# Optimization experiments

Hardware: AMD Instinct MI355X
Metric: run time of the kernel (lower is better)

Reference implementation:

```python
import jax, jax.numpy as jnp
import numpy as np

B, C, T = 128, 9, 2048
R = T // 4            # reduced_timesteps after two MaxPool1d(2)
N = B * R             # total graph nodes
E_SINGLE = 8192       # edges per sample graph (avg degree 16 over R nodes)
HID = 128
OUT = 12


def setup_inputs():
    key = jax.random.key(0)
    ks = jax.random.split(key, 14)
    x = jax.random.normal(ks[0], (B, C, T), jnp.float32)
    # per-sample graph, replicated with offset i*R per batch element (as in forward)
    single = jax.random.randint(ks[1], (2, E_SINGLE), 0, R)
    offsets = (jnp.arange(B) * R)[None, :, None]
    edge_index = (single[:, None, :] + offsets).reshape(2, -1)  # [2, B*E_SINGLE]

    def lin(k, fan_in, shape):
        return jax.random.normal(k, shape, jnp.float32) / np.sqrt(fan_in)

    return {
        "x": x,
        "edge_index": edge_index,
        "conv1_w": lin(ks[2], C * 5, (16, C, 5)),
        "conv1_b": jnp.zeros((16,), jnp.float32),
        "conv2_w": lin(ks[3], 16 * 5, (32, 16, 5)),
        "conv2_b": jnp.zeros((32,), jnp.float32),
        "gcn1_w": lin(ks[4], 32, (32, HID)),
        "gcn1_b": jnp.zeros((HID,), jnp.float32),
        "gcn2_w": lin(ks[5], HID, (HID, HID)),
        "gcn2_b": jnp.zeros((HID,), jnp.float32),
        "fc_w": lin(ks[6], HID, (HID, OUT)),
        "fc_b": jnp.zeros((OUT,), jnp.float32),
    }


def _gcn_conv(h, edge_index, w, b, n):
    # PyG GCNConv: linear -> add self-loops -> sym-normalized sum aggregation -> + bias
    h = h @ w
    loops = jnp.arange(n)
    row = jnp.concatenate([edge_index[0], loops])  # source
    col = jnp.concatenate([edge_index[1], loops])  # target (aggregation)
    deg = jax.ops.segment_sum(jnp.ones(col.shape, h.dtype), col, num_segments=n)
    dis = jnp.where(deg > 0, jax.lax.rsqrt(jnp.maximum(deg, 1e-12)), 0.0)
    norm = dis[row] * dis[col]                      # [E+N]
    out = jax.ops.segment_sum(norm[:, None] * h[row], col, num_segments=n)
    return out + b


def _temporal_conv(x, w1, b1, w2, b2):
    dn = ("NCH", "OIH", "NCH")
    h = jax.lax.conv_general_dilated(x, w1, (1,), [(2, 2)], dimension_numbers=dn)
    h = jax.nn.relu(h + b1[None, :, None])
    h = jax.lax.reduce_window(h, -jnp.inf, jax.lax.max, (1, 1, 2), (1, 1, 2), "VALID")
    h = jax.lax.conv_general_dilated(h, w2, (1,), [(2, 2)], dimension_numbers=dn)
    h = jax.nn.relu(h + b2[None, :, None])
    h = jax.lax.reduce_window(h, -jnp.inf, jax.lax.max, (1, 1, 2), (1, 1, 2), "VALID")
    return h  # [B, 32, R]


def reference(x, edge_index, conv1_w, conv1_b, conv2_w, conv2_b,
              gcn1_w, gcn1_b, gcn2_w, gcn2_b, fc_w, fc_b):
    h = _temporal_conv(x, conv1_w, conv1_b, conv2_w, conv2_b)   # [B, 32, R]
    nodes = h.transpose(0, 2, 1).reshape(B * R, 32)             # [N, 32]
    g = jax.nn.relu(_gcn_conv(nodes, edge_index, gcn1_w, gcn1_b, N))
    g = jax.nn.relu(_gcn_conv(g, edge_index, gcn2_w, gcn2_b, N))
    g = g.reshape(B, R, HID).mean(axis=1)                       # [B, HID]
    return g @ fc_w + fc_b                                      # [B, OUT]
```

## Files before the change

kernel.cpp:

```cpp
#include <hip/hip_runtime.h>
#include <hip/hip_bf16.h>

#define BB   128
#define CIN  9
#define TT   2048
#define RR   512
#define NN   (BB*RR)
#define HID  128
#define NOUT 12

typedef __attribute__((ext_vector_type(8))) short short8;
typedef __attribute__((ext_vector_type(4))) float f32x4;

static __device__ inline unsigned short f2bf(float f) {
    unsigned int u = __float_as_uint(f);
    unsigned int r = (u + 0x7fffu + ((u >> 16) & 1u)) >> 16;
    return (unsigned short)r;
}
static __device__ inline float bf2f(unsigned short u) {
    return __uint_as_float(((unsigned int)u) << 16);
}

__global__ __launch_bounds__(512) void k_convs(const float* __restrict__ x,
        const float* __restrict__ w1, const float* __restrict__ b1,
        const float* __restrict__ w2, const float* __restrict__ b2,
        float* __restrict__ nodes,
        const int* __restrict__ ei, int E, int es,
        int* __restrict__ rptr, float* __restrict__ dis, int* __restrict__ adj) {
    __shared__ float sx[CIN][268];
    __shared__ float s1[16][132];
    __shared__ int lcnt[512];
    __shared__ int sp[512];
    __shared__ int lcur[512];
    int tid = threadIdx.x;

    if (blockIdx.x == 0) {
        int t = tid;
        lcnt[t] = 0;
        __syncthreads();
        for (int i = t; i < es; i += 512) atomicAdd(&lcnt[ei[E + i]], 1);
        __syncthreads();
        int c = lcnt[t];
        sp[t] = c;
        __syncthreads();
        for (int off = 1; off < 512; off <<= 1) {
            int v = sp[t];
            int add = (t >= off) ? sp[t - off] : 0;
            __syncthreads();
            sp[t] = v + add;
            __syncthreads();
        }
        int excl = sp[t] - c;
        rptr[t] = excl;
        if (t == 511) rptr[512] = es;
        dis[t] = rsqrtf((float)c + 1.0f);
        lcur[t] = excl;
        __syncthreads();
        for (int i = t; i < es; i += 512) {
            int row = ei[i], col = ei[E + i];
            int pos = atomicAdd(&lcur[col], 1);
            adj[pos] = row;
        }
        return;
    }

    int cb = blockIdx.x - 1;
    int b  = cb >> 3;
    int r0 = (cb & 7) * 64;
    int wv   = __builtin_amdgcn_readfirstlane(tid >> 6);
    int lane = tid & 63;

    for (int idx = tid; idx < CIN * 268; idx += 512) {
        int c = idx / 268, j = idx - c * 268;
        int g = 4 * r0 - 6 + j;
        float v = 0.f;
        if (g >= 0 && g < TT) v = x[(b * CIN + c) * TT + g];
        sx[c][j] = v;
    }
    __syncthreads();

    {
        int c1a = wv * 2, c1b = wv * 2 + 1;
        float biasA = b1[c1a], biasB = b1[c1b];
        for (int pp = lane; pp < 132; pp += 64) {
            int p = 2 * r0 - 2 + pp;
            float valA = 0.f, valB = 0.f;
            if (p >= 0 && p < 1024) {
                float a0A = biasA, a1A = biasA, a0B = biasB, a1B = biasB;
#pragma unroll
                for (int c = 0; c < CIN; ++c) {
                    const float2* px = (const float2*)&sx[c][2 * pp];
                    float2 q0 = px[0], q1 = px[1], q2 = px[2];
                    {
                        const float* wp = &w1[(c1a * CIN + c) * 5];
                        float k0 = wp[0], k1 = wp[1], k2 = wp[2], k3 = wp[3], k4 = wp[4];
                        a0A += q0.x*k0 + q0.y*k1 + q1.x*k2 + q1.y*k3 + q2.x*k4;
                        a1A += q0.y*k0 + q1.x*k1 + q1.y*k2 + q2.x*k3 + q2.y*k4;
                    }
                    {
                        const float* wp = &w1[(c1b * CIN + c) * 5];
                        float k0 = wp[0], k1 = wp[1], k2 = wp[2], k3 = wp[3], k4 = wp[4];
                        a0B += q0.x*k0 + q0.y*k1 + q1.x*k2 + q1.y*k3 + q2.x*k4;
                        a1B += q0.y*k0 + q1.x*k1 + q1.y*k2 + q2.x*k3 + q2.y*k4;
                    }
                }
                valA = fmaxf(fmaxf(a0A, a1A), 0.f);
                valB = fmaxf(fmaxf(a0B, a1B), 0.f);
            }
            s1[c1a][pp] = valA;
            s1[c1b][pp] = valB;
        }
    }
    __syncthreads();

    int rl = lane;
    float acc0[4], acc1[4];
#pragma unroll
    for (int o = 0; o < 4; ++o) {
        float bv = b2[wv * 4 + o];
        acc0[o] = bv; acc1[o] = bv;
    }
#pragma unroll
    for (int c = 0; c < 16; ++c) {
        const float2* ps = (const float2*)&s1[c][2 * rl];
        float2 q0 = ps[0], q1 = ps[1], q2 = ps[2];
#pragma unroll
        for (int o = 0; o < 4; ++o) {
            const float* wp = &w2[((wv * 4 + o) * 16 + c) * 5];
            float k0 = wp[0], k1 = wp[1], k2 = wp[2], k3 = wp[3], k4 = wp[4];
            acc0[o] += q0.x*k0 + q0.y*k1 + q1.x*k2 + q1.y*k3 + q2.x*k4;
            acc1[o] += q0.y*k0 + q1.x*k1 + q1.y*k2 + q2.x*k3 + q2.y*k4;
        }
    }
    int n = b * RR + r0 + rl;
    float4 ov;
    ov.x = fmaxf(fmaxf(acc0[0], acc1[0]), 0.f);
    ov.y = fmaxf(fmaxf(acc0[1], acc1[1]), 0.f);
    ov.z = fmaxf(fmaxf(acc0[2], acc1[2]), 0.f);
    ov.w = fmaxf(fmaxf(acc0[3], acc1[3]), 0.f);
    *(float4*)&nodes[n * 32 + wv * 4] = ov;
}

__global__ __launch_bounds__(256) void k_gl1(const int* __restrict__ rptr,
        const int* __restrict__ adj, const float* __restrict__ dis,
        const float* __restrict__ nodes, const float* __restrict__ w,
        const float* __restrict__ bias, unsigned short* __restrict__ h16) {
    __shared__ float srow[32][32];
    __shared__ float sw[32 * 128];
    int bid = (blockIdx.x & 7) * 256 + (blockIdx.x >> 3);
    int tid = threadIdx.x;
    int nbase = bid * 32;
    int b = nbase >> 9;
    const float* hb = nodes + (size_t)b * RR * 32;

    {
        const float4* src = (const float4*)w;
        float4* dst = (float4*)sw;
#pragma unroll
        for (int i = 0; i < 4; ++i) dst[tid + i * 256] = src[tid + i * 256];
    }

    int ln   = tid >> 3;
    int lane = tid & 7;
    int r = (nbase & 511) + ln;
    int s = rptr[r], e = rptr[r + 1];
    float dn = dis[r];
    float4 acc = make_float4(0.f, 0.f, 0.f, 0.f);
    for (int base = s; base < e; base += 8) {
        int j = base + lane;
        int src = 0; float nd = 0.f;
        if (j < e) { src = adj[j]; nd = dis[src]; }
        int cnt = min(8, e - base);
        int k = 0;
        for (; k + 4 <= cnt; k += 4) {
            int   s0 = __shfl(src, k, 8),     s1 = __shfl(src, k + 1, 8);
            int   s2 = __shfl(src, k + 2, 8), s3 = __shfl(src, k + 3, 8);
            float n0 = __shfl(nd, k, 8),      n1 = __shfl(nd, k + 1, 8);
            float n2 = __shfl(nd, k + 2, 8),  n3 = __shfl(nd, k + 3, 8);
            float4 v0 = *(const float4*)&hb[(size_t)s0 * 32 + lane * 4];
            float4 v1 = *(const float4*)&hb[(size_t)s1 * 32 + lane * 4];
            float4 v2 = *(const float4*)&hb[(size_t)s2 * 32 + lane * 4];
            float4 v3 = *(const float4*)&hb[(size_t)s3 * 32 + lane * 4];
            float w0 = dn * n0, w1 = dn * n1, w2 = dn * n2, w3 = dn * n3;
            acc.x += w0*v0.x + w1*v1.x + w2*v2.x + w3*v3.x;
            acc.y += w0*v0.y + w1*v1.y + w2*v2.y + w3*v3.y;
            acc.z += w0*v0.z + w1*v1.z + w2*v2.z + w3*v3.z;
            acc.w += w0*v0.w + w1*v1.w + w2*v2.w + w3*v3.w;
        }
        for (; k < cnt; ++k) {
            int   sk = __shfl(src, k, 8);
            float nk = __shfl(nd, k, 8);
            float4 v = *(const float4*)&hb[(size_t)sk * 32 + lane * 4];
            float wgt = dn * nk;
            acc.x += wgt * v.x; acc.y += wgt * v.y;
            acc.z += wgt * v.z; acc.w += wgt * v.w;
        }
    }
    {
        float4 v = *(const float4*)&hb[(size_t)r * 32 + lane * 4];
        float wgt = dn * dn;
        acc.x += wgt * v.x; acc.y += wgt * v.y;
        acc.z += wgt * v.z; acc.w += wgt * v.w;
    }
    *(float4*)&srow[ln][lane * 4] = acc;
    __syncthreads();

    int fq = tid & 31;
    int ng = tid >> 5;
    float a[4][4];
#pragma unroll
    for (int j = 0; j < 4; ++j)
#pragma unroll
        for (int q = 0; q < 4; ++q) a[j][q] = 0.f;
#pragma unroll
    for (int c = 0; c < 32; ++c) {
        float4 wvv = *(const float4*)&sw[c * 128 + fq * 4];
#pragma unroll
        for (int j = 0; j < 4; ++j) {
            float xc = srow[ng * 4 + j][c];
            a[j][0] += xc * wvv.x; a[j][1] += xc * wvv.y;
            a[j][2] += xc * wvv.z; a[j][3] += xc * wvv.w;
        }
    }
    float4 bv = *(const float4*)&bias[fq * 4];
#pragma unroll
    for (int j = 0; j < 4; ++j) {
        ushort4 o;
        o.x = f2bf(fmaxf(a[j][0] + bv.x, 0.f));
        o.y = f2bf(fmaxf(a[j][1] + bv.y, 0.f));
        o.z = f2bf(fmaxf(a[j][2] + bv.z, 0.f));
        o.w = f2bf(fmaxf(a[j][3] + bv.w, 0.f));
        *(ushort4*)&h16[(size_t)(nbase + ng * 4 + j) * 128 + fq * 4] = o;
    }
}

__global__ __launch_bounds__(256) void k_lin2(const unsigned short* __restrict__ g16,
        const float* __restrict__ w, unsigned short* __restrict__ h16) {
    __shared__ unsigned short srow[64][136];
    __shared__ unsigned short swT[128][136];
    int tid = threadIdx.x;
    int nbase = blockIdx.x * 64;

    {
        const ushort4* src = (const ushort4*)(g16 + (size_t)nbase * 128);
#pragma unroll
        for (int i = 0; i < 8; ++i) {
            int idx = tid + i * 256;
            int row = idx >> 5, col4 = idx & 31;
            ushort4 v = src[idx];
            *(ushort4*)&srow[row][col4 * 4] = v;
        }
    }
    {
        for (int i = 0; i < 64; ++i) {
            int idx = i * 256 + tid;
            int c = idx >> 7, f = idx & 127;
            swT[f][c] = f2bf(w[idx]);
        }
    }
    __syncthreads();

    int wv  = tid >> 6;
    int lane = tid & 63;
    int m0 = wv * 16;
    int l15 = lane & 15;
    int quad = lane >> 4;
    f32x4 acc[8];
#pragma unroll
    for (int nt = 0; nt < 8; ++nt) acc[nt] = (f32x4){0.f, 0.f, 0.f, 0.f};
#pragma unroll
    for (int kc = 0; kc < 4; ++kc) {
        int k0 = kc * 32 + quad * 8;
        short8 a = *(const short8*)&srow[m0 + l15][k0];
#pragma unroll
        for (int nt = 0; nt < 8; ++nt) {
            short8 b = *(const short8*)&swT[nt * 16 + l15][k0];
            acc[nt] = __builtin_amdgcn_mfma_f32_16x16x32_bf16(a, b, acc[nt], 0, 0, 0);
        }
    }
#pragma unroll
    for (int nt = 0; nt < 8; ++nt) {
#pragma unroll
        for (int r = 0; r < 4; ++r) {
            int row = m0 + quad * 4 + r;
            int col = nt * 16 + l15;
            h16[(size_t)(nbase + row) * 128 + col] = f2bf(acc[nt][r]);
        }
    }
}

__global__ __launch_bounds__(256) void k_gather128(const int* __restrict__ rptr,
        const int* __restrict__ adj, const float* __restrict__ dis,
        const unsigned short* __restrict__ h, const float* __restrict__ bias,
        float* __restrict__ partial) {
    __shared__ float sred[8][128];
    int bid  = (blockIdx.x & 7) * 1024 + (blockIdx.x >> 3);
    int tid  = threadIdx.x;
    int g    = tid >> 5;
    int lane = tid & 31;
    int node = bid * 8 + g;
    int b = node >> 9;
    int r = node & 511;
    const unsigned short* hb = h + (size_t)b * RR * 128;
    int s = rptr[r], e = rptr[r + 1];
    float dn = dis[r];
    float4 acc = make_float4(0.f, 0.f, 0.f, 0.f);
    for (int base = s; base < e; base += 32) {
        int j = base + lane;
        int src = 0; float nd = 0.f;
        if (j < e) { src = adj[j]; nd = dis[src]; }
        int cnt = min(32, e - base);
        int k = 0;
        for (; k + 4 <= cnt; k += 4) {
            int   s0 = __shfl(src, k, 32),     s1 = __shfl(src, k + 1, 32);
            int   s2 = __shfl(src, k + 2, 32), s3 = __shfl(src, k + 3, 32);
            float n0 = __shfl(nd, k, 32),      n1 = __shfl(nd, k + 1, 32);
            float n2 = __shfl(nd, k + 2, 32),  n3 = __shfl(nd, k + 3, 32);
            ushort4 u0 = *(const ushort4*)&hb[(size_t)s0 * 128 + lane * 4];
            ushort4 u1 = *(const ushort4*)&hb[(size_t)s1 * 128 + lane * 4];
            ushort4 u2 = *(const ushort4*)&hb[(size_t)s2 * 128 + lane * 4];
            ushort4 u3 = *(const ushort4*)&hb[(size_t)s3 * 128 + lane * 4];
            float w0 = dn * n0, w1 = dn * n1, w2 = dn * n2, w3 = dn * n3;
            acc.x += w0*bf2f(u0.x) + w1*bf2f(u1.x) + w2*bf2f(u2.x) + w3*bf2f(u3.x);
            acc.y += w0*bf2f(u0.y) + w1*bf2f(u1.y) + w2*bf2f(u2.y) + w3*bf2f(u3.y);
            acc.z += w0*bf2f(u0.z) + w1*bf2f(u1.z) + w2*bf2f(u2.z) + w3*bf2f(u3.z);
            acc.w += w0*bf2f(u0.w) + w1*bf2f(u1.w) + w2*bf2f(u2.w) + w3*bf2f(u3.w);
        }
        for (; k < cnt; ++k) {
            int   sk = __shfl(src, k, 32);
            float nk = __shfl(nd, k, 32);
            ushort4 u = *(const ushort4*)&hb[(size_t)sk * 128 + lane * 4];
            float wgt = dn * nk;
            acc.x += wgt * bf2f(u.x); acc.y += wgt * bf2f(u.y);
            acc.z += wgt * bf2f(u.z); acc.w += wgt * bf2f(u.w);
        }
    }
    ushort4 u = *(const ushort4*)&hb[(size_t)r * 128 + lane * 4];
    float wgt = dn * dn;
    float4 bv = *(const float4*)&bias[lane * 4];
    acc.x = fmaxf(acc.x + wgt * bf2f(u.x) + bv.x, 0.f);
    acc.y = fmaxf(acc.y + wgt * bf2f(u.y) + bv.y, 0.f);
    acc.z = fmaxf(acc.z + wgt * bf2f(u.z) + bv.z, 0.f);
    acc.w = fmaxf(acc.w + wgt * bf2f(u.w) + bv.w, 0.f);
    *(float4*)&sred[g][lane * 4] = acc;
    __syncthreads();
    if (tid < 128) {
        float ssum = 0.f;
#pragma unroll
        for (int j = 0; j < 8; ++j) ssum += sred[j][tid];
        partial[(size_t)bid * 128 + tid] = ssum;
    }
}

__global__ __launch_bounds__(128) void k_fc(const float* __restrict__ partial,
        const float* __restrict__ fw, const float* __restrict__ fb,
        float* __restrict__ out) {
    __shared__ float sm[HID];
    int b = blockIdx.x, f = threadIdx.x;
    float acc = 0.f;
#pragma unroll 8
    for (int j = 0; j < 64; ++j) acc += partial[(size_t)(b * 64 + j) * 128 + f];
    sm[f] = acc * (1.0f / RR);
    __syncthreads();
    if (f < NOUT) {
        float s = fb[f];
#pragma unroll
        for (int c = 0; c < HID; ++c) s += sm[c] * fw[c * NOUT + f];
        out[b * NOUT + f] = s;
    }
}

extern "C" void kernel_launch(void* const* d_in, const int* in_sizes, int n_in,
                              void* d_out, int out_size, void* d_ws, size_t ws_size,
                              hipStream_t stream) {
    const float* x   = (const float*)d_in[0];
    const int*   ei  = (const int*)d_in[1];
    const float* c1w = (const float*)d_in[2];
    const float* c1b = (const float*)d_in[3];
    const float* c2w = (const float*)d_in[4];
    const float* c2b = (const float*)d_in[5];
    const float* g1w = (const float*)d_in[6];
    const float* g1b = (const float*)d_in[7];
    const float* g2w = (const float*)d_in[8];
    const float* g2b = (const float*)d_in[9];
    const float* fw  = (const float*)d_in[10];
    const float* fb  = (const float*)d_in[11];
    float* out = (float*)d_out;
    int E  = in_sizes[1] / 2;
    int es = E / BB;

    char* ws = (char*)d_ws;
    float*          nodes   = (float*)(ws);
    unsigned short* bufA16  = (unsigned short*)(ws + (8u  << 20));
    unsigned short* bufC16  = (unsigned short*)(ws + (24u << 20));
    int*   rptr    = (int*)  (ws + (40u << 20));
    float* dis     = (float*)(ws + (40u << 20) + 4096);
    int*   adj     = (int*)  (ws + (40u << 20) + 8192);
    float* partial = (float*)(ws + (41u << 20));

    k_convs<<<BB * 8 + 1, 512, 0, stream>>>(x, c1w, c1b, c2w, c2b, nodes,
                                            ei, E, es, rptr, dis, adj);

    k_gl1<<<NN / 32, 256, 0, stream>>>(rptr, adj, dis, nodes, g1w, g1b, bufA16);

    k_lin2<<<NN / 64, 256, 0, stream>>>(bufA16, g2w, bufC16);
    k_gather128<<<NN / 8, 256, 0, stream>>>(rptr, adj, dis, bufC16, g2b, partial);

    k_fc<<<BB, 128, 0, stream>>>(partial, fw, fb, out);
}
```

Baseline: 172.9 us.

## Fuse GCN layer-2 linear into layer-1 kernel and store conv nodes in bf16

Merges the separate layer-2 linear kernel into the layer-1 aggregate+linear kernel. The 32-node layer-1 outputs stay in shared memory and feed bf16 MFMAs directly, which removes a full N×128 bf16 round trip through global memory and one launch. The second-layer weight is transposed to bf16 once, in the graph-building block of the conv kernel. Conv outputs are now stored as bf16, halving gather traffic for layer 1, at some cost in precision. The layer-2 gather loop also gets an 8-wide unroll, and the MFMA B operand is read from global memory (L2) rather than LDS.

```diff
diff --git a/kernel.cpp b/kernel.cpp
--- a/kernel.cpp
+++ b/kernel.cpp
@@ -21,12 +21,15 @@
     return __uint_as_float(((unsigned int)u) << 16);
 }
 
+#define MFMA16(a, b, c) __builtin_amdgcn_mfma_f32_16x16x32_bf16((a), (b), (c), 0, 0, 0)
+
 __global__ __launch_bounds__(512) void k_convs(const float* __restrict__ x,
         const float* __restrict__ w1, const float* __restrict__ b1,
         const float* __restrict__ w2, const float* __restrict__ b2,
-        float* __restrict__ nodes,
+        unsigned short* __restrict__ nodes16,
         const int* __restrict__ ei, int E, int es,
-        int* __restrict__ rptr, float* __restrict__ dis, int* __restrict__ adj) {
+        int* __restrict__ rptr, float* __restrict__ dis, int* __restrict__ adj,
+        const float* __restrict__ g2w, unsigned short* __restrict__ w2t) {
     __shared__ float sx[CIN][268];
     __shared__ float s1[16][132];
     __shared__ int lcnt[512];
@@ -60,6 +63,10 @@
             int row = ei[i], col = ei[E + i];
             int pos = atomicAdd(&lcur[col], 1);
             adj[pos] = row;
+        }
+        for (int idx = t; idx < 128 * 128; idx += 512) {
+            int c2 = idx >> 7, f = idx & 127;
+            w2t[f * 128 + c2] = f2bf(g2w[idx]);
         }
         return;
     }
@@ -133,25 +140,27 @@
         }
     }
     int n = b * RR + r0 + rl;
-    float4 ov;
-    ov.x = fmaxf(fmaxf(acc0[0], acc1[0]), 0.f);
-    ov.y = fmaxf(fmaxf(acc0[1], acc1[1]), 0.f);
-    ov.z = fmaxf(fmaxf(acc0[2], acc1[2]), 0.f);
-    ov.w = fmaxf(fmaxf(acc0[3], acc1[3]), 0.f);
-    *(float4*)&nodes[n * 32 + wv * 4] = ov;
-}
-
-__global__ __launch_bounds__(256) void k_gl1(const int* __restrict__ rptr,
+    ushort4 ov;
+    ov.x = f2bf(fmaxf(fmaxf(acc0[0], acc1[0]), 0.f));
+    ov.y = f2bf(fmaxf(fmaxf(acc0[1], acc1[1]), 0.f));
+    ov.z = f2bf(fmaxf(fmaxf(acc0[2], acc1[2]), 0.f));
+    ov.w = f2bf(fmaxf(fmaxf(acc0[3], acc1[3]), 0.f));
+    *(ushort4*)&nodes16[n * 32 + wv * 4] = ov;
+}
+
+__global__ __launch_bounds__(256) void k_gl12(const int* __restrict__ rptr,
         const int* __restrict__ adj, const float* __restrict__ dis,
-        const float* __restrict__ nodes, const float* __restrict__ w,
-        const float* __restrict__ bias, unsigned short* __restrict__ h16) {
+        const unsigned short* __restrict__ nodes16, const float* __restrict__ w,
+        const float* __restrict__ bias, const unsigned short* __restrict__ w2t,
+        unsigned short* __restrict__ h2out) {
+    __shared__ float sw[32 * 128];
     __shared__ float srow[32][32];
-    __shared__ float sw[32 * 128];
+    __shared__ unsigned short sh1[32][136];
     int bid = (blockIdx.x & 7) * 256 + (blockIdx.x >> 3);
     int tid = threadIdx.x;
     int nbase = bid * 32;
     int b = nbase >> 9;
-    const float* hb = nodes + (size_t)b * RR * 32;
+    const unsigned short* hb = nodes16 + (size_t)b * RR * 32;
 
     {
         const float4* src = (const float4*)w;
@@ -160,14 +169,14 @@
         for (int i = 0; i < 4; ++i) dst[tid + i * 256] = src[tid + i * 256];
     }
 
-    int ln   = tid >> 3;
-    int lane = tid & 7;
+    int ln    = tid >> 3;
+    int lane8 = tid & 7;
     int r = (nbase & 511) + ln;
     int s = rptr[r], e = rptr[r + 1];
     float dn = dis[r];
     float4 acc = make_float4(0.f, 0.f, 0.f, 0.f);
     for (int base = s; base < e; base += 8) {
-        int j = base + lane;
+        int j = base + lane8;
         int src = 0; float nd = 0.f;
         if (j < e) { src = adj[j]; nd = dis[src]; }
         int cnt = min(8, e - base);
@@ -177,114 +186,93 @@
             int   s2 = __shfl(src, k + 2, 8), s3 = __shfl(src, k + 3, 8);
             float n0 = __shfl(nd, k, 8),      n1 = __shfl(nd, k + 1, 8);
             float n2 = __shfl(nd, k + 2, 8),  n3 = __shfl(nd, k + 3, 8);
-            float4 v0 = *(const float4*)&hb[(size_t)s0 * 32 + lane * 4];
-            float4 v1 = *(const float4*)&hb[(size_t)s1 * 32 + lane * 4];
-            float4 v2 = *(const float4*)&hb[(size_t)s2 * 32 + lane * 4];
-            float4 v3 = *(const float4*)&hb[(size_t)s3 * 32 + lane * 4];
+            ushort4 u0 = *(const ushort4*)&hb[(size_t)s0 * 32 + lane8 * 4];
+            ushort4 u1 = *(const ushort4*)&hb[(size_t)s1 * 32 + lane8 * 4];
+            ushort4 u2 = *(const ushort4*)&hb[(size_t)s2 * 32 + lane8 * 4];
+            ushort4 u3 = *(const ushort4*)&hb[(size_t)s3 * 32 + lane8 * 4];
             float w0 = dn * n0, w1 = dn * n1, w2 = dn * n2, w3 = dn * n3;
-            acc.x += w0*v0.x + w1*v1.x + w2*v2.x + w3*v3.x;
-            acc.y += w0*v0.y + w1*v1.y + w2*v2.y + w3*v3.y;
-            acc.z += w0*v0.z + w1*v1.z + w2*v2.z + w3*v3.z;
-            acc.w += w0*v0.w + w1*v1.w + w2*v2.w + w3*v3.w;
+            acc.x += w0*bf2f(u0.x) + w1*bf2f(u1.x) + w2*bf2f(u2.x) + w3*bf2f(u3.x);
+            acc.y += w0*bf2f(u0.y) + w1*bf2f(u1.y) + w2*bf2f(u2.y) + w3*bf2f(u3.y);
+            acc.z += w0*bf2f(u0.z) + w1*bf2f(u1.z) + w2*bf2f(u2.z) + w3*bf2f(u3.z);
+            acc.w += w0*bf2f(u0.w) + w1*bf2f(u1.w) + w2*bf2f(u2.w) + w3*bf2f(u3.w);
         }
         for (; k < cnt; ++k) {
             int   sk = __shfl(src, k, 8);
             float nk = __shfl(nd, k, 8);
-            float4 v = *(const float4*)&hb[(size_t)sk * 32 + lane * 4];
+            ushort4 u = *(const ushort4*)&hb[(size_t)sk * 32 + lane8 * 4];
             float wgt = dn * nk;
-            acc.x += wgt * v.x; acc.y += wgt * v.y;
-            acc.z += wgt * v.z; acc.w += wgt * v.w;
+            acc.x += wgt * bf2f(u.x); acc.y += wgt * bf2f(u.y);
+            acc.z += wgt * bf2f(u.z); acc.w += wgt * bf2f(u.w);
         }
     }
     {
-        float4 v = *(const float4*)&hb[(size_t)r * 32 + lane * 4];
+        ushort4 u = *(const ushort4*)&hb[(size_t)r * 32 + lane8 * 4];
         float wgt = dn * dn;
-        acc.x += wgt * v.x; acc.y += wgt * v.y;
-        acc.z += wgt * v.z; acc.w += wgt * v.w;
-    }
-    *(float4*)&srow[ln][lane * 4] = acc;
-    __syncthreads();
-
-    int fq = tid & 31;
-    int ng = tid >> 5;
-    float a[4][4];
-#pragma unroll
-    for (int j = 0; j < 4; ++j)
-#pragma unroll
-        for (int q = 0; q < 4; ++q) a[j][q] = 0.f;
-#pragma unroll
-    for (int c = 0; c < 32; ++c) {
-        float4 wvv = *(const float4*)&sw[c * 128 + fq * 4];
+        acc.x += wgt * bf2f(u.x); acc.y += wgt * bf2f(u.y);
+        acc.z += wgt * bf2f(u.z); acc.w += wgt * bf2f(u.w);
+    }
+    *(float4*)&srow[ln][lane8 * 4] = acc;
+    __syncthreads();
+
+    {
+        int fq = tid & 31;
+        int ng = tid >> 5;
+        float a[4][4];
+#pragma unroll
+        for (int j = 0; j < 4; ++j)
+#pragma unroll
+            for (int q = 0; q < 4; ++q) a[j][q] = 0.f;
+#pragma unroll
+        for (int c = 0; c < 32; ++c) {
+            float4 wvv = *(const float4*)&sw[c * 128 + fq * 4];
+#pragma unroll
+            for (int j = 0; j < 4; ++j) {
+                float xc = srow[ng * 4 + j][c];
+                a[j][0] += xc * wvv.x; a[j][1] += xc * wvv.y;
+                a[j][2] += xc * wvv.z; a[j][3] += xc * wvv.w;
+            }
+        }
+        float4 bv = *(const float4*)&bias[fq * 4];
 #pragma unroll
         for (int j = 0; j < 4; ++j) {
-            float xc = srow[ng * 4 + j][c];
-            a[j][0] += xc * wvv.x; a[j][1] += xc * wvv.y;
-            a[j][2] += xc * wvv.z; a[j][3] += xc * wvv.w;
-        }
-    }
-    float4 bv = *(const float4*)&bias[fq * 4];
-#pragma unroll
-    for (int j = 0; j < 4; ++j) {
-        ushort4 o;
-        o.x = f2bf(fmaxf(a[j][0] + bv.x, 0.f));
-        o.y = f2bf(fmaxf(a[j][1] + bv.y, 0.f));
-        o.z = f2bf(fmaxf(a[j][2] + bv.z, 0.f));
-        o.w = f2bf(fmaxf(a[j][3] + bv.w, 0.f));
-        *(ushort4*)&h16[(size_t)(nbase + ng * 4 + j) * 128 + fq * 4] = o;
-    }
-}
-
-__global__ __launch_bounds__(256) void k_lin2(const unsigned short* __restrict__ g16,
-        const float* __restrict__ w, unsigned short* __restrict__ h16) {
-    __shared__ unsigned short srow[64][136];
-    __shared__ unsigned short swT[128][136];
-    int tid = threadIdx.x;
-    int nbase = blockIdx.x * 64;
+            ushort4 o;
+            o.x = f2bf(fmaxf(a[j][0] + bv.x, 0.f));
+            o.y = f2bf(fmaxf(a[j][1] + bv.y, 0.f));
+            o.z = f2bf(fmaxf(a[j][2] + bv.z, 0.f));
+            o.w = f2bf(fmaxf(a[j][3] + bv.w, 0.f));
+            *(ushort4*)&sh1[ng * 4 + j][fq * 4] = o;
+        }
+    }
+    __syncthreads();
 
     {
-        const ushort4* src = (const ushort4*)(g16 + (size_t)nbase * 128);
-#pragma unroll
-        for (int i = 0; i < 8; ++i) {
-            int idx = tid + i * 256;
-            int row = idx >> 5, col4 = idx & 31;
-            ushort4 v = src[idx];
-            *(ushort4*)&srow[row][col4 * 4] = v;
-        }
-    }
-    {
-        for (int i = 0; i < 64; ++i) {
-            int idx = i * 256 + tid;
-            int c = idx >> 7, f = idx & 127;
-            swT[f][c] = f2bf(w[idx]);
-        }
-    }
-    __syncthreads();
-
-    int wv  = tid >> 6;
-    int lane = tid & 63;
-    int m0 = wv * 16;
-    int l15 = lane & 15;
-    int quad = lane >> 4;
-    f32x4 acc[8];
-#pragma unroll
-    for (int nt = 0; nt < 8; ++nt) acc[nt] = (f32x4){0.f, 0.f, 0.f, 0.f};
-#pragma unroll
-    for (int kc = 0; kc < 4; ++kc) {
-        int k0 = kc * 32 + quad * 8;
-        short8 a = *(const short8*)&srow[m0 + l15][k0];
-#pragma unroll
-        for (int nt = 0; nt < 8; ++nt) {
-            short8 b = *(const short8*)&swT[nt * 16 + l15][k0];
-            acc[nt] = __builtin_amdgcn_mfma_f32_16x16x32_bf16(a, b, acc[nt], 0, 0, 0);
-        }
-    }
-#pragma unroll
-    for (int nt = 0; nt < 8; ++nt) {
-#pragma unroll
-        for (int r = 0; r < 4; ++r) {
-            int row = m0 + quad * 4 + r;
-            int col = nt * 16 + l15;
-            h16[(size_t)(nbase + row) * 128 + col] = f2bf(acc[nt][r]);
+        int wv   = tid >> 6;
+        int lane = tid & 63;
+        int l15  = lane & 15;
+        int quad = lane >> 4;
+        int m0 = (wv & 1) * 16;
+        int nh = wv >> 1;
+        f32x4 acc2[4];
+#pragma unroll
+        for (int nt = 0; nt < 4; ++nt) acc2[nt] = (f32x4){0.f, 0.f, 0.f, 0.f};
+#pragma unroll
+        for (int kc = 0; kc < 4; ++kc) {
+            short8 a = *(const short8*)&sh1[m0 + l15][kc * 32 + quad * 8];
+#pragma unroll
+            for (int nt = 0; nt < 4; ++nt) {
+                int col0 = nh * 64 + nt * 16;
+                short8 bfr = *(const short8*)&w2t[(size_t)(col0 + l15) * 128 + kc * 32 + quad * 8];
+                acc2[nt] = MFMA16(a, bfr, acc2[nt]);
+            }
+        }
+#pragma unroll
+        for (int nt = 0; nt < 4; ++nt) {
+            int col = nh * 64 + nt * 16 + l15;
+#pragma unroll
+            for (int rr2 = 0; rr2 < 4; ++rr2) {
+                int row = nbase + m0 + quad * 4 + rr2;
+                h2out[(size_t)row * 128 + col] = f2bf(acc2[nt][rr2]);
+            }
         }
     }
 }
@@ -311,6 +299,25 @@
         if (j < e) { src = adj[j]; nd = dis[src]; }
         int cnt = min(32, e - base);
         int k = 0;
+        for (; k + 8 <= cnt; k += 8) {
+#pragma unroll
+            for (int uu = 0; uu < 2; ++uu) {
+                int kk = k + uu * 4;
+                int   s0 = __shfl(src, kk, 32),     s1 = __shfl(src, kk + 1, 32);
+                int   s2 = __shfl(src, kk + 2, 32), s3 = __shfl(src, kk + 3, 32);
+                float n0 = __shfl(nd, kk, 32),      n1 = __shfl(nd, kk + 1, 32);
+                float n2 = __shfl(nd, kk + 2, 32),  n3 = __shfl(nd, kk + 3, 32);
+                ushort4 u0 = *(const ushort4*)&hb[(size_t)s0 * 128 + lane * 4];
+                ushort4 u1 = *(const ushort4*)&hb[(size_t)s1 * 128 + lane * 4];
+                ushort4 u2 = *(const ushort4*)&hb[(size_t)s2 * 128 + lane * 4];
+                ushort4 u3 = *(const ushort4*)&hb[(size_t)s3 * 128 + lane * 4];
+                float w0 = dn * n0, w1 = dn * n1, w2 = dn * n2, w3 = dn * n3;
+                acc.x += w0*bf2f(u0.x) + w1*bf2f(u1.x) + w2*bf2f(u2.x) + w3*bf2f(u3.x);
+                acc.y += w0*bf2f(u0.y) + w1*bf2f(u1.y) + w2*bf2f(u2.y) + w3*bf2f(u3.y);
+                acc.z += w0*bf2f(u0.z) + w1*bf2f(u1.z) + w2*bf2f(u2.z) + w3*bf2f(u3.z);
+                acc.w += w0*bf2f(u0.w) + w1*bf2f(u1.w) + w2*bf2f(u2.w) + w3*bf2f(u3.w);
+            }
+        }
         for (; k + 4 <= cnt; k += 4) {
             int   s0 = __shfl(src, k, 32),     s1 = __shfl(src, k + 1, 32);
             int   s2 = __shfl(src, k + 2, 32), s3 = __shfl(src, k + 3, 32);
@@ -390,20 +397,19 @@
     int es = E / BB;
 
     char* ws = (char*)d_ws;
-    float*          nodes   = (float*)(ws);
-    unsigned short* bufA16  = (unsigned short*)(ws + (8u  << 20));
-    unsigned short* bufC16  = (unsigned short*)(ws + (24u << 20));
-    int*   rptr    = (int*)  (ws + (40u << 20));
-    float* dis     = (float*)(ws + (40u << 20) + 4096);
-    int*   adj     = (int*)  (ws + (40u << 20) + 8192);
-    float* partial = (float*)(ws + (41u << 20));
-
-    k_convs<<<BB * 8 + 1, 512, 0, stream>>>(x, c1w, c1b, c2w, c2b, nodes,
-                                            ei, E, es, rptr, dis, adj);
-
-    k_gl1<<<NN / 32, 256, 0, stream>>>(rptr, adj, dis, nodes, g1w, g1b, bufA16);
-
-    k_lin2<<<NN / 64, 256, 0, stream>>>(bufA16, g2w, bufC16);
+    unsigned short* nodes16 = (unsigned short*)(ws);
+    unsigned short* bufC16  = (unsigned short*)(ws + (4u << 20));
+    int*   rptr    = (int*)  (ws + (20u << 20));
+    float* dis     = (float*)(ws + (20u << 20) + 4096);
+    int*   adj     = (int*)  (ws + (20u << 20) + 8192);
+    unsigned short* w2t = (unsigned short*)(ws + (20u << 20) + 65536);
+    float* partial = (float*)(ws + (21u << 20));
+
+    k_convs<<<BB * 8 + 1, 512, 0, stream>>>(x, c1w, c1b, c2w, c2b, nodes16,
+                                            ei, E, es, rptr, dis, adj, g2w, w2t);
+
+    k_gl12<<<NN / 32, 256, 0, stream>>>(rptr, adj, dis, nodes16, g1w, g1b, w2t, bufC16);
+
     k_gather128<<<NN / 8, 256, 0, stream>>>(rptr, adj, dis, bufC16, g2b, partial);
 
     k_fc<<<BB, 128, 0, stream>>>(partial, fw, fb, out);
```

New measurement: 179.8 us. 1.04x slower.
